# Performance work log

Measured on AMD Instinct MI355X. Metric: run time of the kernel, lower is better.

Reference implementation:

```python
import jax, jax.numpy as jnp
import numpy as np

N, DEG, F_IN, F_OUT = 100000, 16, 128, 128
E = N * DEG


def setup_inputs() -> dict:
    key = jax.random.key(0)
    k0, k1, k2, k3 = jax.random.split(key, 4)
    x = jax.random.normal(k0, (N, F_IN), dtype=jnp.float32)
    # ragged neighbor list flattened: each node has DEG neighbors (sorted segment ids)
    neighbor_feats = jax.random.normal(k1, (E, F_IN), dtype=jnp.float32)
    segment_ids = jnp.repeat(jnp.arange(N, dtype=jnp.int32), DEG)
    # nn.Linear(in, out, bias=False) weights, stored [out, in] as in torch
    Wx = jax.random.normal(k2, (F_OUT, F_IN), dtype=jnp.float32) / np.float32(np.sqrt(F_IN))
    Wn = jax.random.normal(k3, (F_OUT, F_IN), dtype=jnp.float32) / np.float32(np.sqrt(F_IN))
    return {"x": x, "neighbor_feats": neighbor_feats, "segment_ids": segment_ids,
            "Wx": Wx, "Wn": Wn}


def reference(x, neighbor_feats, segment_ids, Wx, Wn):
    n_nodes = x.shape[0]
    # MeanAggregator: per-node mean over its neighbor rows (segment mean)
    sums = jax.ops.segment_sum(neighbor_feats, segment_ids, num_segments=n_nodes)
    counts = jax.ops.segment_sum(
        jnp.ones((neighbor_feats.shape[0],), dtype=x.dtype), segment_ids,
        num_segments=n_nodes)
    f = sums / jnp.maximum(counts, 1.0)[:, None]  # [N, F_IN]
    # tranx(x) + trann(f)
    x_out = x @ Wx.T + f @ Wn.T                   # [N, F_OUT]
    # neighbor = [tranx(n) for n in neighbor], flattened
    nb_out = neighbor_feats @ Wx.T                # [E, F_OUT]
    return x_out, nb_out
```

## Files before the change

kernel.cpp:

```cpp
#include <hip/hip_runtime.h>
#include <stdint.h>
#include <stddef.h>

#define N_NODES 100000
#define F_DIM   128
#define DEG     16
#define N_EDGES (N_NODES*DEG)
#define ROWS_PER_TILE 128
#define N_TILES (N_EDGES/ROWS_PER_TILE)
#define NODES_PER_TILE (ROWS_PER_TILE/DEG)
#define GRID_BLOCKS 2500
#define TILES_PER_BLOCK (N_TILES/GRID_BLOCKS)
#define BLOCK_THREADS 256
#define G_STRIDE 132

typedef __bf16 bf16;
typedef __bf16 bf16x8 __attribute__((ext_vector_type(8)));
typedef float  f32x4  __attribute__((ext_vector_type(4)));

__device__ __forceinline__ int swz(int row, int col) {
  return row*128 + (col ^ ((row & 7) << 3));
}

__device__ __forceinline__ bf16x8 cvt8(f32x4 a, f32x4 b) {
  bf16x8 v;
  v[0]=(bf16)a[0]; v[1]=(bf16)a[1]; v[2]=(bf16)a[2]; v[3]=(bf16)a[3];
  v[4]=(bf16)b[0]; v[5]=(bf16)b[1]; v[6]=(bf16)b[2]; v[7]=(bf16)b[3];
  return v;
}

__device__ __forceinline__ bf16x8 load_frag_g(const float* __restrict__ p) {
  f32x4 a = *(const f32x4*)p;
  f32x4 b = *(const f32x4*)(p + 4);
  return cvt8(a, b);
}

__global__ __launch_bounds__(BLOCK_THREADS, 2)
void feattrans_kernel(const float* __restrict__ x,
                      const float* __restrict__ nb,
                      const float* __restrict__ Wx,
                      const float* __restrict__ Wn,
                      float* __restrict__ out)
{
  __shared__ bf16  w_lds[2*128*128];
  __shared__ float g_lds[2][NODES_PER_TILE][G_STRIDE];

  const int tid  = threadIdx.x;
  const int wave = tid >> 6;
  const int lane = tid & 63;
  const int l15  = lane & 15;
  const int lk   = lane >> 4;

  #pragma unroll
  for (int it = 0; it < 16; ++it) {
    int idx = it * BLOCK_THREADS + tid;
    int mat = idx >> 11;
    int rem = idx & 2047;
    int row = rem >> 4;
    int g   = rem & 15;
    const float* src = (mat ? Wn : Wx) + row*128 + g*8;
    bf16x8 v = load_frag_g(src);
    *(bf16x8*)&w_lds[mat*16384 + swz(row, g*8)] = v;
  }
  __syncthreads();

  float* out_x  = out;
  float* out_nb = out + (size_t)N_NODES * F_DIM;

  const int bid = blockIdx.x;

  bf16x8 afr[2][2][4];

  {
    const size_t erow0 = (size_t)bid * ROWS_PER_TILE;
    #pragma unroll
    for (int mt = 0; mt < 2; ++mt)
      #pragma unroll
      for (int ks = 0; ks < 4; ++ks)
        afr[0][mt][ks] = load_frag_g(nb + (erow0 + wave*32 + mt*16 + l15) * F_DIM + ks*32 + lk*8);
  }

  #pragma unroll
  for (int t = 0; t < TILES_PER_BLOCK; ++t) {
    const int cur = t & 1, nxt = cur ^ 1;
    const int tile = bid + t * GRID_BLOCKS;
    const size_t erow0 = (size_t)tile * ROWS_PER_TILE;
    const int nodebase = tile * NODES_PER_TILE;

    const int xrow = nodebase + (l15 & 7);
    bf16x8 xfr[4];
    #pragma unroll
    for (int ks = 0; ks < 4; ++ks)
      xfr[ks] = load_frag_g(x + (size_t)xrow * F_DIM + ks*32 + lk*8);

    f32x4 acc[2][8] = {};
    #pragma unroll
    for (int nt = 0; nt < 8; ++nt) {
      #pragma unroll
      for (int ks = 0; ks < 4; ++ks) {
        bf16x8 bfr = *(bf16x8*)&w_lds[swz(nt*16 + l15, ks*32 + lk*8)];
        acc[0][nt] = __builtin_amdgcn_mfma_f32_16x16x32_bf16(bfr, afr[cur][0][ks], acc[0][nt], 0, 0, 0);
        acc[1][nt] = __builtin_amdgcn_mfma_f32_16x16x32_bf16(bfr, afr[cur][1][ks], acc[1][nt], 0, 0, 0);
      }
    }
    #pragma unroll
    for (int mt = 0; mt < 2; ++mt)
      #pragma unroll
      for (int nt = 0; nt < 8; ++nt)
        *(f32x4*)(out_nb + (erow0 + wave*32 + mt*16 + l15) * F_DIM + nt*16 + lk*4) = acc[mt][nt];

    f32x4 a2[2][8] = {};
    #pragma unroll
    for (int nt = 0; nt < 8; ++nt) {
      #pragma unroll
      for (int ks = 0; ks < 4; ++ks) {
        bf16x8 bfr = *(bf16x8*)&w_lds[16384 + swz(nt*16 + l15, ks*32 + lk*8)];
        a2[0][nt] = __builtin_amdgcn_mfma_f32_16x16x32_bf16(afr[cur][0][ks], bfr, a2[0][nt], 0, 0, 0);
        a2[1][nt] = __builtin_amdgcn_mfma_f32_16x16x32_bf16(afr[cur][1][ks], bfr, a2[1][nt], 0, 0, 0);
      }
    }
    #pragma unroll
    for (int mt = 0; mt < 2; ++mt) {
      const int gnode = 2*wave + mt;
      #pragma unroll
      for (int nt = 0; nt < 8; ++nt) {
        float s = a2[mt][nt][0] + a2[mt][nt][1] + a2[mt][nt][2] + a2[mt][nt][3];
        s += __shfl_xor(s, 16, 64);
        s += __shfl_xor(s, 32, 64);
        s *= (1.0f / DEG);
        if (lk == (nt >> 1))
          g_lds[cur][gnode][nt*16 + l15] = s;
      }
    }

    if (t < TILES_PER_BLOCK - 1) {
      const size_t erowN = erow0 + (size_t)GRID_BLOCKS * ROWS_PER_TILE;
      #pragma unroll
      for (int mt = 0; mt < 2; ++mt)
        #pragma unroll
        for (int ks = 0; ks < 4; ++ks)
          afr[nxt][mt][ks] = load_frag_g(nb + (erowN + wave*32 + mt*16 + l15) * F_DIM + ks*32 + lk*8);
    }

    __syncthreads();

    f32x4 xacc[2] = {};
    #pragma unroll
    for (int j = 0; j < 2; ++j) {
      const int nt = 2*wave + j;
      #pragma unroll
      for (int ks = 0; ks < 4; ++ks) {
        bf16x8 bx = *(bf16x8*)&w_lds[swz(nt*16 + l15, ks*32 + lk*8)];
        xacc[j] = __builtin_amdgcn_mfma_f32_16x16x32_bf16(bx, xfr[ks], xacc[j], 0, 0, 0);
      }
    }
    if (l15 < NODES_PER_TILE) {
      #pragma unroll
      for (int j = 0; j < 2; ++j) {
        const int nt = 2*wave + j;
        f32x4 g4 = *(f32x4*)&g_lds[cur][l15][nt*16 + lk*4];
        f32x4 v  = xacc[j] + g4;
        *(f32x4*)(out_x + (size_t)(nodebase + l15) * F_DIM + nt*16 + lk*4) = v;
      }
    }
  }
}

extern "C" void kernel_launch(void* const* d_in, const int* in_sizes, int n_in,
                              void* d_out, int out_size, void* d_ws, size_t ws_size,
                              hipStream_t stream) {
  const float* x  = (const float*)d_in[0];
  const float* nb = (const float*)d_in[1];
  const float* Wx = (const float*)d_in[3];
  const float* Wn = (const float*)d_in[4];
  float* out = (float*)d_out;

  feattrans_kernel<<<dim3(GRID_BLOCKS), dim3(BLOCK_THREADS), 0, stream>>>(x, nb, Wx, Wn, out);
}
```

Baseline: 354.5 us.

## Move Wn out of LDS to a bf16 global copy to raise occupancy

Wn is converted to bf16 once into workspace by a small pre-kernel. The main kernel now reads its B fragments straight from global memory (through the cache) instead of LDS. This halves the LDS footprint, and the launch bounds are raised from 2 to 3 blocks per SM so more blocks can be resident and hide memory latency. The cost is extra global/L2 traffic in the inner MFMA loop and an additional kernel launch; a fallback path converts fp32 Wn on the fly when no workspace is available.

```diff
diff --git a/kernel.cpp b/kernel.cpp
--- a/kernel.cpp
+++ b/kernel.cpp
@@ -35,14 +35,24 @@
   return cvt8(a, b);
 }
 
-__global__ __launch_bounds__(BLOCK_THREADS, 2)
+__global__ void wn_to_bf16_kernel(const float* __restrict__ Wn, bf16* __restrict__ wn) {
+  const int idx = blockIdx.x * blockDim.x + threadIdx.x;
+  const float* src = Wn + (size_t)idx * 8;
+  f32x4 a = *(const f32x4*)src;
+  f32x4 b = *(const f32x4*)(src + 4);
+  *(bf16x8*)&wn[(size_t)idx * 8] = cvt8(a, b);
+}
+
+template <bool WS>
+__global__ __launch_bounds__(BLOCK_THREADS, 3)
 void feattrans_kernel(const float* __restrict__ x,
                       const float* __restrict__ nb,
                       const float* __restrict__ Wx,
-                      const float* __restrict__ Wn,
+                      const bf16*  __restrict__ wn,
+                      const float* __restrict__ WnF,
                       float* __restrict__ out)
 {
-  __shared__ bf16  w_lds[2*128*128];
+  __shared__ bf16  w_lds[128*128];
   __shared__ float g_lds[2][NODES_PER_TILE][G_STRIDE];
 
   const int tid  = threadIdx.x;
@@ -52,15 +62,13 @@
   const int lk   = lane >> 4;
 
   #pragma unroll
-  for (int it = 0; it < 16; ++it) {
+  for (int it = 0; it < 8; ++it) {
     int idx = it * BLOCK_THREADS + tid;
-    int mat = idx >> 11;
-    int rem = idx & 2047;
-    int row = rem >> 4;
-    int g   = rem & 15;
-    const float* src = (mat ? Wn : Wx) + row*128 + g*8;
+    int row = idx >> 4;
+    int g   = idx & 15;
+    const float* src = Wx + row*128 + g*8;
     bf16x8 v = load_frag_g(src);
-    *(bf16x8*)&w_lds[mat*16384 + swz(row, g*8)] = v;
+    *(bf16x8*)&w_lds[swz(row, g*8)] = v;
   }
   __syncthreads();
 
@@ -114,7 +122,12 @@
     for (int nt = 0; nt < 8; ++nt) {
       #pragma unroll
       for (int ks = 0; ks < 4; ++ks) {
-        bf16x8 bfr = *(bf16x8*)&w_lds[16384 + swz(nt*16 + l15, ks*32 + lk*8)];
+        bf16x8 bfr;
+        if constexpr (WS) {
+          bfr = *(const bf16x8*)&wn[(size_t)(nt*16 + l15) * 128 + ks*32 + lk*8];
+        } else {
+          bfr = load_frag_g(WnF + (size_t)(nt*16 + l15) * 128 + ks*32 + lk*8);
+        }
         a2[0][nt] = __builtin_amdgcn_mfma_f32_16x16x32_bf16(afr[cur][0][ks], bfr, a2[0][nt], 0, 0, 0);
         a2[1][nt] = __builtin_amdgcn_mfma_f32_16x16x32_bf16(afr[cur][1][ks], bfr, a2[1][nt], 0, 0, 0);
       }
@@ -175,5 +188,13 @@
   const float* Wn = (const float*)d_in[4];
   float* out = (float*)d_out;
 
-  feattrans_kernel<<<dim3(GRID_BLOCKS), dim3(BLOCK_THREADS), 0, stream>>>(x, nb, Wx, Wn, out);
-}
+  if (ws_size >= (size_t)(128*128) * sizeof(bf16)) {
+    bf16* wn = (bf16*)d_ws;
+    wn_to_bf16_kernel<<<dim3(8), dim3(256), 0, stream>>>(Wn, wn);
+    feattrans_kernel<true><<<dim3(GRID_BLOCKS), dim3(BLOCK_THREADS), 0, stream>>>(
+        x, nb, Wx, wn, Wn, out);
+  } else {
+    feattrans_kernel<false><<<dim3(GRID_BLOCKS), dim3(BLOCK_THREADS), 0, stream>>>(
+        x, nb, Wx, nullptr, Wn, out);
+  }
+}
```

Result: slower. 696.0 us (+96.3%).

## Split fused kernel into neighbor kernel and separate x-projection kernel via workspace

Applied to the files above, without the earlier changes.

Splits the monolithic kernel into two launches. The first computes the neighbor projections and writes the per-node mean-aggregated Wn term to a workspace buffer. The second computes x@Wx for 128 nodes per block, adds the workspace term and writes x_out. The aim is to drop the per-tile barrier and the poorly utilized 8-row x MFMA from the main loop, at the cost of an extra launch and writing then re-reading a 51 MB intermediate. A fallback to the original fused kernel is kept for when the workspace is too small.

```diff
diff --git a/kernel.cpp b/kernel.cpp
--- a/kernel.cpp
+++ b/kernel.cpp
@@ -36,14 +36,13 @@
 }
 
 __global__ __launch_bounds__(BLOCK_THREADS, 2)
-void feattrans_kernel(const float* __restrict__ x,
-                      const float* __restrict__ nb,
-                      const float* __restrict__ Wx,
-                      const float* __restrict__ Wn,
-                      float* __restrict__ out)
+void feattrans_nb_kernel(const float* __restrict__ nb,
+                         const float* __restrict__ Wx,
+                         const float* __restrict__ Wn,
+                         float* __restrict__ out_nb,
+                         float* __restrict__ g_out)
 {
-  __shared__ bf16  w_lds[2*128*128];
-  __shared__ float g_lds[2][NODES_PER_TILE][G_STRIDE];
+  __shared__ bf16 w_lds[2*128*128];
 
   const int tid  = threadIdx.x;
   const int wave = tid >> 6;
@@ -64,11 +63,164 @@
   }
   __syncthreads();
 
+  const int bid = blockIdx.x;
+  bf16x8 afr[2][2][4];
+
+  {
+    const size_t erow0 = (size_t)bid * ROWS_PER_TILE;
+    #pragma unroll
+    for (int mt = 0; mt < 2; ++mt)
+      #pragma unroll
+      for (int ks = 0; ks < 4; ++ks)
+        afr[0][mt][ks] = load_frag_g(nb + (erow0 + wave*32 + mt*16 + l15) * F_DIM + ks*32 + lk*8);
+  }
+
+  #pragma unroll
+  for (int t = 0; t < TILES_PER_BLOCK; ++t) {
+    const int cur = t & 1, nxt = cur ^ 1;
+    const int tile = bid + t * GRID_BLOCKS;
+    const size_t erow0 = (size_t)tile * ROWS_PER_TILE;
+    const int nodebase = tile * NODES_PER_TILE;
+
+    f32x4 acc[2][8] = {};
+    #pragma unroll
+    for (int nt = 0; nt < 8; ++nt) {
+      #pragma unroll
+      for (int ks = 0; ks < 4; ++ks) {
+        bf16x8 bfr = *(bf16x8*)&w_lds[swz(nt*16 + l15, ks*32 + lk*8)];
+        acc[0][nt] = __builtin_amdgcn_mfma_f32_16x16x32_bf16(bfr, afr[cur][0][ks], acc[0][nt], 0, 0, 0);
+        acc[1][nt] = __builtin_amdgcn_mfma_f32_16x16x32_bf16(bfr, afr[cur][1][ks], acc[1][nt], 0, 0, 0);
+      }
+    }
+    #pragma unroll
+    for (int mt = 0; mt < 2; ++mt)
+      #pragma unroll
+      for (int nt = 0; nt < 8; ++nt)
+        *(f32x4*)(out_nb + (erow0 + wave*32 + mt*16 + l15) * F_DIM + nt*16 + lk*4) = acc[mt][nt];
+
+    f32x4 a2[2][8] = {};
+    #pragma unroll
+    for (int nt = 0; nt < 8; ++nt) {
+      #pragma unroll
+      for (int ks = 0; ks < 4; ++ks) {
+        bf16x8 bfr = *(bf16x8*)&w_lds[16384 + swz(nt*16 + l15, ks*32 + lk*8)];
+        a2[0][nt] = __builtin_amdgcn_mfma_f32_16x16x32_bf16(afr[cur][0][ks], bfr, a2[0][nt], 0, 0, 0);
+        a2[1][nt] = __builtin_amdgcn_mfma_f32_16x16x32_bf16(afr[cur][1][ks], bfr, a2[1][nt], 0, 0, 0);
+      }
+    }
+    #pragma unroll
+    for (int mt = 0; mt < 2; ++mt) {
+      const int gnode = nodebase + 2*wave + mt;
+      #pragma unroll
+      for (int nt = 0; nt < 8; ++nt) {
+        float s = a2[mt][nt][0] + a2[mt][nt][1] + a2[mt][nt][2] + a2[mt][nt][3];
+        s += __shfl_xor(s, 16, 64);
+        s += __shfl_xor(s, 32, 64);
+        s *= (1.0f / DEG);
+        if (lk == (nt >> 1))
+          g_out[(size_t)gnode * F_DIM + nt*16 + l15] = s;
+      }
+    }
+
+    if (t < TILES_PER_BLOCK - 1) {
+      const size_t erowN = erow0 + (size_t)GRID_BLOCKS * ROWS_PER_TILE;
+      #pragma unroll
+      for (int mt = 0; mt < 2; ++mt)
+        #pragma unroll
+        for (int ks = 0; ks < 4; ++ks)
+          afr[nxt][mt][ks] = load_frag_g(nb + (erowN + wave*32 + mt*16 + l15) * F_DIM + ks*32 + lk*8);
+    }
+  }
+}
+
+#define B_ROWS_PER_BLOCK 128
+#define B_GRID ((N_NODES + B_ROWS_PER_BLOCK - 1) / B_ROWS_PER_BLOCK)
+
+__global__ __launch_bounds__(BLOCK_THREADS, 4)
+void feattrans_x_kernel(const float* __restrict__ x,
+                        const float* __restrict__ Wx,
+                        const float* __restrict__ g_in,
+                        float* __restrict__ out_x)
+{
+  __shared__ bf16 w_lds[128*128];
+
+  const int tid  = threadIdx.x;
+  const int wave = tid >> 6;
+  const int lane = tid & 63;
+  const int l15  = lane & 15;
+  const int lk   = lane >> 4;
+
+  #pragma unroll
+  for (int it = 0; it < 8; ++it) {
+    int idx = it * BLOCK_THREADS + tid;
+    int row = idx >> 4;
+    int g   = idx & 15;
+    bf16x8 v = load_frag_g(Wx + row*128 + g*8);
+    *(bf16x8*)&w_lds[swz(row, g*8)] = v;
+  }
+  __syncthreads();
+
+  #pragma unroll
+  for (int i = 0; i < 2; ++i) {
+    const int rbase = blockIdx.x * B_ROWS_PER_BLOCK + wave*32 + i*16;
+    int xrow = rbase + l15;
+    const bool valid = (xrow < N_NODES);
+    if (xrow > N_NODES - 1) xrow = N_NODES - 1;
+
+    bf16x8 xfr[4];
+    #pragma unroll
+    for (int ks = 0; ks < 4; ++ks)
+      xfr[ks] = load_frag_g(x + (size_t)xrow * F_DIM + ks*32 + lk*8);
+
+    #pragma unroll
+    for (int nt = 0; nt < 8; ++nt) {
+      f32x4 xacc = {};
+      #pragma unroll
+      for (int ks = 0; ks < 4; ++ks) {
+        bf16x8 bx = *(bf16x8*)&w_lds[swz(nt*16 + l15, ks*32 + lk*8)];
+        xacc = __builtin_amdgcn_mfma_f32_16x16x32_bf16(bx, xfr[ks], xacc, 0, 0, 0);
+      }
+      if (valid) {
+        f32x4 g4 = *(const f32x4*)&g_in[(size_t)xrow * F_DIM + nt*16 + lk*4];
+        f32x4 v  = xacc + g4;
+        *(f32x4*)(out_x + (size_t)xrow * F_DIM + nt*16 + lk*4) = v;
+      }
+    }
+  }
+}
+
+__global__ __launch_bounds__(BLOCK_THREADS, 2)
+void feattrans_mono_kernel(const float* __restrict__ x,
+                           const float* __restrict__ nb,
+                           const float* __restrict__ Wx,
+                           const float* __restrict__ Wn,
+                           float* __restrict__ out)
+{
+  __shared__ bf16  w_lds[2*128*128];
+  __shared__ float g_lds[2][NODES_PER_TILE][G_STRIDE];
+
+  const int tid  = threadIdx.x;
+  const int wave = tid >> 6;
+  const int lane = tid & 63;
+  const int l15  = lane & 15;
+  const int lk   = lane >> 4;
+
+  #pragma unroll
+  for (int it = 0; it < 16; ++it) {
+    int idx = it * BLOCK_THREADS + tid;
+    int mat = idx >> 11;
+    int rem = idx & 2047;
+    int row = rem >> 4;
+    int g   = rem & 15;
+    const float* src = (mat ? Wn : Wx) + row*128 + g*8;
+    bf16x8 v = load_frag_g(src);
+    *(bf16x8*)&w_lds[mat*16384 + swz(row, g*8)] = v;
+  }
+  __syncthreads();
+
   float* out_x  = out;
   float* out_nb = out + (size_t)N_NODES * F_DIM;
-
   const int bid = blockIdx.x;
-
   bf16x8 afr[2][2][4];
 
   {
@@ -175,5 +327,15 @@
   const float* Wn = (const float*)d_in[4];
   float* out = (float*)d_out;
 
-  feattrans_kernel<<<dim3(GRID_BLOCKS), dim3(BLOCK_THREADS), 0, stream>>>(x, nb, Wx, Wn, out);
-}
+  const size_t g_bytes = (size_t)N_NODES * F_DIM * sizeof(float);
+  if (ws_size >= g_bytes) {
+    float* g_ws = (float*)d_ws;
+    feattrans_nb_kernel<<<dim3(GRID_BLOCKS), dim3(BLOCK_THREADS), 0, stream>>>(
+        nb, Wx, Wn, out + (size_t)N_NODES * F_DIM, g_ws);
+    feattrans_x_kernel<<<dim3(B_GRID), dim3(BLOCK_THREADS), 0, stream>>>(
+        x, Wx, g_ws, out);
+  } else {
+    feattrans_mono_kernel<<<dim3(GRID_BLOCKS), dim3(BLOCK_THREADS), 0, stream>>>(
+        x, nb, Wx, Wn, out);
+  }
+}
```

Result: slower. 382.4 us (+7.9%).

## Compute x projection per wave in-register and drop LDS exchange and barrier

Applied to the files above, without the earlier changes.

Each wave now computes the Wx projection for its own two nodes inside the existing Wx MFMA loop, reusing the loaded B fragments. It then adds the neighbor mean from registers and writes x_out directly. This removes the g_lds shared buffer, the per-tile __syncthreads, and the separate x MFMA pass with its extra LDS reads. In exchange it issues 32 extra MFMAs per wave, most of whose output rows are wasted, and uses narrower scalar stores for x_out.

```diff
diff --git a/kernel.cpp b/kernel.cpp
--- a/kernel.cpp
+++ b/kernel.cpp
@@ -12,7 +12,6 @@
 #define GRID_BLOCKS 2500
 #define TILES_PER_BLOCK (N_TILES/GRID_BLOCKS)
 #define BLOCK_THREADS 256
-#define G_STRIDE 132
 
 typedef __bf16 bf16;
 typedef __bf16 bf16x8 __attribute__((ext_vector_type(8)));
@@ -42,8 +41,7 @@
                       const float* __restrict__ Wn,
                       float* __restrict__ out)
 {
-  __shared__ bf16  w_lds[2*128*128];
-  __shared__ float g_lds[2][NODES_PER_TILE][G_STRIDE];
+  __shared__ bf16 w_lds[2*128*128];
 
   const int tid  = threadIdx.x;
   const int wave = tid >> 6;
@@ -87,13 +85,14 @@
     const size_t erow0 = (size_t)tile * ROWS_PER_TILE;
     const int nodebase = tile * NODES_PER_TILE;
 
-    const int xrow = nodebase + (l15 & 7);
+    const int xrow = nodebase + 2*wave + (l15 & 1);
     bf16x8 xfr[4];
     #pragma unroll
     for (int ks = 0; ks < 4; ++ks)
       xfr[ks] = load_frag_g(x + (size_t)xrow * F_DIM + ks*32 + lk*8);
 
     f32x4 acc[2][8] = {};
+    f32x4 xacc[8] = {};
     #pragma unroll
     for (int nt = 0; nt < 8; ++nt) {
       #pragma unroll
@@ -101,6 +100,7 @@
         bf16x8 bfr = *(bf16x8*)&w_lds[swz(nt*16 + l15, ks*32 + lk*8)];
         acc[0][nt] = __builtin_amdgcn_mfma_f32_16x16x32_bf16(bfr, afr[cur][0][ks], acc[0][nt], 0, 0, 0);
         acc[1][nt] = __builtin_amdgcn_mfma_f32_16x16x32_bf16(bfr, afr[cur][1][ks], acc[1][nt], 0, 0, 0);
+        xacc[nt]   = __builtin_amdgcn_mfma_f32_16x16x32_bf16(xfr[ks], bfr, xacc[nt], 0, 0, 0);
       }
     }
     #pragma unroll
@@ -119,17 +119,24 @@
         a2[1][nt] = __builtin_amdgcn_mfma_f32_16x16x32_bf16(afr[cur][1][ks], bfr, a2[1][nt], 0, 0, 0);
       }
     }
+    float g[2][8];
     #pragma unroll
     for (int mt = 0; mt < 2; ++mt) {
-      const int gnode = 2*wave + mt;
       #pragma unroll
       for (int nt = 0; nt < 8; ++nt) {
         float s = a2[mt][nt][0] + a2[mt][nt][1] + a2[mt][nt][2] + a2[mt][nt][3];
         s += __shfl_xor(s, 16, 64);
         s += __shfl_xor(s, 32, 64);
-        s *= (1.0f / DEG);
-        if (lk == (nt >> 1))
-          g_lds[cur][gnode][nt*16 + l15] = s;
+        g[mt][nt] = s * (1.0f / DEG);
+      }
+    }
+
+    if (lk == 0) {
+      #pragma unroll
+      for (int nt = 0; nt < 8; ++nt) {
+        #pragma unroll
+        for (int i = 0; i < 2; ++i)
+          out_x[(size_t)(nodebase + 2*wave + i) * F_DIM + nt*16 + l15] = xacc[nt][i] + g[i][nt];
       }
     }
 
@@ -140,28 +147,6 @@
         #pragma unroll
         for (int ks = 0; ks < 4; ++ks)
           afr[nxt][mt][ks] = load_frag_g(nb + (erowN + wave*32 + mt*16 + l15) * F_DIM + ks*32 + lk*8);
-    }
-
-    __syncthreads();
-
-    f32x4 xacc[2] = {};
-    #pragma unroll
-    for (int j = 0; j < 2; ++j) {
-      const int nt = 2*wave + j;
-      #pragma unroll
-      for (int ks = 0; ks < 4; ++ks) {
-        bf16x8 bx = *(bf16x8*)&w_lds[swz(nt*16 + l15, ks*32 + lk*8)];
-        xacc[j] = __builtin_amdgcn_mfma_f32_16x16x32_bf16(bx, xfr[ks], xacc[j], 0, 0, 0);
-      }
-    }
-    if (l15 < NODES_PER_TILE) {
-      #pragma unroll
-      for (int j = 0; j < 2; ++j) {
-        const int nt = 2*wave + j;
-        f32x4 g4 = *(f32x4*)&g_lds[cur][l15][nt*16 + lk*4];
-        f32x4 v  = xacc[j] + g4;
-        *(f32x4*)(out_x + (size_t)(nodebase + l15) * F_DIM + nt*16 + lk*4) = v;
-      }
     }
   }
 }
```

New measurement: 341.2 us, median of 2. -3.8%, faster.
